# Performance work log

Measured on AMD Instinct MI355X. Metric: run time of the kernel, lower is better.

## Reference

```python
import jax, jax.numpy as jnp
import numpy as np

B, D_MODEL, SEQ = 8, 1024, 1024   # D_MODEL = hidden_dim*2
H, DK, DV = 8, 128, 128
EPS_LN, EPS_NORM, NEG = 1e-6, 1e-12, -1e9


def layer_norm_2d(x, g, b):
    # torch LayerNorm([d_model, seq_len]): normalize over last two dims
    mu = jnp.mean(x, axis=(-2, -1), keepdims=True)
    var = jnp.mean((x - mu) ** 2, axis=(-2, -1), keepdims=True)
    return (x - mu) * jax.lax.rsqrt(var + EPS_LN) * g + b


def setup_inputs() -> dict:
    key = jax.random.key(0)
    ks = jax.random.split(key, 14)
    s = lambda *sh: 1.0 / np.sqrt(sh[-1])
    return {
        "enc_input": jax.random.normal(ks[0], (B, D_MODEL, SEQ), jnp.float32),
        "slf_attn_mask": jax.random.randint(ks[1], (B, D_MODEL, D_MODEL), 0, 2, jnp.int32),
        "ln1_g": jnp.ones((D_MODEL, SEQ), jnp.float32),
        "ln1_b": jnp.zeros((D_MODEL, SEQ), jnp.float32),
        "wq": jax.random.normal(ks[2], (H * DK, SEQ), jnp.float32) * s(SEQ),
        "wk": jax.random.normal(ks[3], (H * DK, SEQ), jnp.float32) * s(SEQ),
        "wv": jax.random.normal(ks[4], (H * DV, SEQ), jnp.float32) * s(SEQ),
        "wo": jax.random.normal(ks[5], (SEQ, H * DV), jnp.float32) * s(H * DV),
        "ln2_g": jnp.ones((D_MODEL, SEQ), jnp.float32),
        "ln2_b": jnp.zeros((D_MODEL, SEQ), jnp.float32),
        "w1": jax.random.normal(ks[6], (SEQ, SEQ), jnp.float32) * s(SEQ),
        "b1": jnp.zeros((SEQ,), jnp.float32),
        "w2": jax.random.normal(ks[7], (SEQ, SEQ), jnp.float32) * s(SEQ),
        "b2": jnp.zeros((SEQ,), jnp.float32),
    }


def reference(enc_input, slf_attn_mask, ln1_g, ln1_b, wq, wk, wv, wo,
              ln2_g, ln2_b, w1, b1, w2, b2):
    x = enc_input                                # [B, M, S], M = d_model
    residual = x
    h = layer_norm_2d(x, ln1_g, ln1_b)
    # linear projections on last (seq) dim, split heads -> [B, H, M, dk]
    q = jnp.einsum('bms,os->bmo', h, wq).reshape(B, D_MODEL, H, DK).transpose(0, 2, 1, 3)
    k = jnp.einsum('bms,os->bmo', h, wk).reshape(B, D_MODEL, H, DK).transpose(0, 2, 1, 3)
    v = jnp.einsum('bms,os->bmo', h, wv).reshape(B, D_MODEL, H, DV).transpose(0, 2, 1, 3)
    # F.normalize over dim=1 (the HEAD axis) -- faithful to source
    k_norm = k / jnp.maximum(jnp.sqrt(jnp.sum(k * k, axis=1, keepdims=True)), EPS_NORM)
    # no temperature scaling (stored but unused in source)
    attn = jnp.einsum('bhmd,bhnd->bhmn', q, k_norm)          # [B, H, M, M]
    attn = jnp.where(slf_attn_mask[:, None] == 0, NEG, attn)
    attn = jax.nn.softmax(attn, axis=-1)
    out = jnp.einsum('bhmn,bhnd->bhmd', attn, v)             # [B, H, M, dv]
    out = out.transpose(0, 2, 1, 3).reshape(B, D_MODEL, H * DV)
    x = jnp.einsum('bmo,so->bms', out, wo) + residual        # fc + residual
    # positionwise FFN on the seq axis, pre-LN residual
    h2 = layer_norm_2d(x, ln2_g, ln2_b)
    h2 = jax.nn.relu(jnp.einsum('bms,os->bmo', h2, w1) + b1)
    h2 = jnp.einsum('bmo,so->bms', h2, w2) + b2
    enc_output = h2 + x
    return enc_output, attn
```

## Files before the change

### kernel.cpp

```cpp
#include <hip/hip_runtime.h>

#define DEVINL __device__ __forceinline__

typedef __bf16 bf16x8 __attribute__((ext_vector_type(8)));
typedef float  f32x4  __attribute__((ext_vector_type(4)));

DEVINL unsigned short f2bf(float f) {
  union { float f; unsigned int u; } v; v.f = f;
  unsigned int u = v.u;
  return (unsigned short)((u + 0x7fffu + ((u >> 16) & 1u)) >> 16);
}
DEVINL float bf2f(unsigned short b) {
  union { unsigned int u; float f; } v; v.u = ((unsigned int)b) << 16;
  return v.f;
}
DEVINL __bf16 fbf(float f) {
  unsigned short u = f2bf(f);
  return __builtin_bit_cast(__bf16, u);
}

#define GLD_LDS16(SRC, DST) \
  __builtin_amdgcn_global_load_lds((const __attribute__((address_space(1))) void*)(SRC), \
                                   (__attribute__((address_space(3))) void*)(DST), 16, 0, 0)

template<int EPI, bool AF32>
__global__ __launch_bounds__(256) void gemm_bt(
    const void* __restrict__ Ap, const unsigned short* __restrict__ Bp, void* __restrict__ Cp,
    const float* __restrict__ bias, const float* __restrict__ res,
    int M, int N, int K, int lda, int ldb, int ldc, int H,
    long sAb, long sAh, long sBb, long sBh, long sCb, long sCh)
{
  constexpr int ABYTES = AF32 ? 16384 : 8192;
  constexpr int SMEMSZ = (EPI == 2) ? 34816 : (ABYTES + 8192);
  __shared__ __align__(16) char smem[SMEMSZ];
  unsigned short* sB = (unsigned short*)(smem + ABYTES);

  const int tid = threadIdx.x;
  const int w = tid >> 6, l = tid & 63;
  const int wr = w >> 1, wc = w & 1;
  const int ntn = N >> 7;
  const int tm = (int)blockIdx.x / ntn;
  const int tn = (int)blockIdx.x - tm * ntn;
  const int z = blockIdx.z;
  const int bb = z / H, hh = z - bb * H;
  const long offA = (long)bb * sAb + (long)hh * sAh;
  const long offB = (long)bb * sBb + (long)hh * sBh;
  const long offC = (long)bb * sCb + (long)hh * sCh;

  f32x4 zero = {0.f, 0.f, 0.f, 0.f};
  f32x4 acc[4][4];
  #pragma unroll
  for (int m = 0; m < 4; ++m)
    #pragma unroll
    for (int n = 0; n < 4; ++n) acc[m][n] = zero;

  for (int k0 = 0; k0 < K; k0 += 32) {
    __syncthreads();
    if constexpr (!AF32) {
      const unsigned short* A = (const unsigned short*)Ap;
      const int rl = l >> 2, cl = (l & 3) << 3;
      #pragma unroll
      for (int i = 0; i < 2; ++i) {
        const unsigned short* src = A + offA + (long)(tm*128 + w*32 + i*16 + rl) * lda + (k0 + cl);
        unsigned short* dst = (unsigned short*)smem + (w*32 + i*16) * 32;
        GLD_LDS16(src, dst);
      }
    } else {
      const float* A = (const float*)Ap;
      const int rl = l >> 3, cl = (l & 7) << 2;
      #pragma unroll
      for (int i = 0; i < 4; ++i) {
        const float* src = A + offA + (long)(tm*128 + w*32 + i*8 + rl) * lda + (k0 + cl);
        float* dst = (float*)smem + (w*32 + i*8) * 32;
        GLD_LDS16(src, dst);
      }
    }
    {
      const int rl = l >> 2, cl = (l & 3) << 3;
      #pragma unroll
      for (int i = 0; i < 2; ++i) {
        const unsigned short* src = Bp + offB + (long)(tn*128 + w*32 + i*16 + rl) * ldb + (k0 + cl);
        unsigned short* dst = sB + (w*32 + i*16) * 32;
        GLD_LDS16(src, dst);
      }
    }
    __syncthreads();

    bf16x8 af[4], bfr[4];
    if constexpr (!AF32) {
      const unsigned short* sA = (const unsigned short*)smem;
      #pragma unroll
      for (int m = 0; m < 4; ++m) {
        int row = wr*64 + m*16 + (l & 15);
        af[m] = *(const bf16x8*)(sA + row*32 + ((l >> 4) << 3));
      }
    } else {
      const float* sA = (const float*)smem;
      #pragma unroll
      for (int m = 0; m < 4; ++m) {
        int row = wr*64 + m*16 + (l & 15);
        const float* p = sA + row*32 + ((l >> 4) << 3);
        f32x4 v0 = *(const f32x4*)p;
        f32x4 v1 = *(const f32x4*)(p + 4);
        bf16x8 t;
        t[0]=fbf(v0[0]); t[1]=fbf(v0[1]); t[2]=fbf(v0[2]); t[3]=fbf(v0[3]);
        t[4]=fbf(v1[0]); t[5]=fbf(v1[1]); t[6]=fbf(v1[2]); t[7]=fbf(v1[3]);
        af[m] = t;
      }
    }
    #pragma unroll
    for (int n = 0; n < 4; ++n) {
      int row = wc*64 + n*16 + (l & 15);
      bfr[n] = *(const bf16x8*)(sB + row*32 + ((l >> 4) << 3));
    }
    #pragma unroll
    for (int m = 0; m < 4; ++m)
      #pragma unroll
      for (int n = 0; n < 4; ++n)
        acc[m][n] = __builtin_amdgcn_mfma_f32_16x16x32_bf16(af[m], bfr[n], acc[m][n], 0, 0, 0);
  }

  if constexpr (EPI == 2) {
    __syncthreads();
    unsigned short* sT = (unsigned short*)smem;
    #pragma unroll
    for (int m = 0; m < 4; ++m)
      #pragma unroll
      for (int n = 0; n < 4; ++n)
        #pragma unroll
        for (int r = 0; r < 4; ++r) {
          int rowl = wr*64 + m*16 + ((l >> 4) << 2) + r;
          int coll = wc*64 + n*16 + (l & 15);
          sT[coll*136 + rowl] = f2bf(acc[m][n][r]);
        }
    __syncthreads();
    #pragma unroll
    for (int i = 0; i < 8; ++i) {
      int idx = tid + i*256;
      int c = idx >> 4, ch = idx & 15;
      bf16x8 vv = *(const bf16x8*)(sT + c*136 + ch*8);
      *(bf16x8*)((unsigned short*)Cp + offC + (long)(tn*128 + c)*ldc + (tm*128 + ch*8)) = vv;
    }
  } else {
    #pragma unroll
    for (int m = 0; m < 4; ++m) {
      #pragma unroll
      for (int n = 0; n < 4; ++n) {
        #pragma unroll
        for (int r = 0; r < 4; ++r) {
          int row = tm*128 + wr*64 + m*16 + ((l >> 4) << 2) + r;
          int col = tn*128 + wc*64 + n*16 + (l & 15);
          float v = acc[m][n][r];
          long ci = offC + (long)row * ldc + col;
          if constexpr (EPI == 1) {
            ((unsigned short*)Cp)[ci] = f2bf(v);
          } else if constexpr (EPI == 3) {
            ((float*)Cp)[ci] = v + res[ci];
          } else if constexpr (EPI == 4) {
            ((unsigned short*)Cp)[ci] = f2bf(fmaxf(v + bias[col], 0.f));
          } else if constexpr (EPI == 5) {
            ((float*)Cp)[ci] = v + bias[col] + res[ci];
          }
        }
      }
    }
  }
}

template<int EPI>
__global__ __launch_bounds__(256) void gemm_split(
    const unsigned short* __restrict__ A1, const unsigned short* __restrict__ A2,
    const unsigned short* __restrict__ B1, const unsigned short* __restrict__ B2,
    void* __restrict__ Cp, unsigned short* __restrict__ Cp2,
    int M, int N, int K, int lda, int ldb, int ldc, int H,
    long sAb, long sAh, long sBb, long sBh, long sCb, long sCh)
{
  __shared__ __align__(16) unsigned short sAll[4 * 4096];
  unsigned short* sA1 = sAll;
  unsigned short* sA2 = sAll + 4096;
  unsigned short* sB1 = sAll + 8192;
  unsigned short* sB2 = sAll + 12288;

  const int tid = threadIdx.x;
  const int w = tid >> 6, l = tid & 63;
  const int wr = w >> 1, wc = w & 1;
  const int ntn = N >> 7;
  const int tm = (int)blockIdx.x / ntn;
  const int tn = (int)blockIdx.x - tm * ntn;
  const int z = blockIdx.z;
  const int bb = z / H, hh = z - bb * H;
  const long offA = (long)bb * sAb + (long)hh * sAh;
  const long offB = (long)bb * sBb + (long)hh * sBh;
  const long offC = (long)bb * sCb + (long)hh * sCh;

  f32x4 zero = {0.f, 0.f, 0.f, 0.f};
  f32x4 acc[4][4];
  #pragma unroll
  for (int m = 0; m < 4; ++m)
    #pragma unroll
    for (int n = 0; n < 4; ++n) acc[m][n] = zero;

  const int rl = l >> 2, cl = (l & 3) << 3;

  for (int k0 = 0; k0 < K; k0 += 32) {
    __syncthreads();
    #pragma unroll
    for (int i = 0; i < 2; ++i) {
      const int row = w*32 + i*16;
      const long asrc = offA + (long)(tm*128 + row + rl) * lda + (k0 + cl);
      const long bsrc = offB + (long)(tn*128 + row + rl) * ldb + (k0 + cl);
      GLD_LDS16(A1 + asrc, sA1 + row*32);
      GLD_LDS16(A2 + asrc, sA2 + row*32);
      GLD_LDS16(B1 + bsrc, sB1 + row*32);
      GLD_LDS16(B2 + bsrc, sB2 + row*32);
    }
    __syncthreads();

    bf16x8 a1[4], a2[4], bb4[4];
    int aoff[4], boff[4];
    #pragma unroll
    for (int m = 0; m < 4; ++m) {
      int row = wr*64 + m*16 + (l & 15);
      aoff[m] = row*32 + ((l >> 4) << 3);
      a1[m] = *(const bf16x8*)(sA1 + aoff[m]);
      a2[m] = *(const bf16x8*)(sA2 + aoff[m]);
    }
    #pragma unroll
    for (int n = 0; n < 4; ++n) {
      int row = wc*64 + n*16 + (l & 15);
      boff[n] = row*32 + ((l >> 4) << 3);
      bb4[n] = *(const bf16x8*)(sB1 + boff[n]);
    }
    #pragma unroll
    for (int m = 0; m < 4; ++m)
      #pragma unroll
      for (int n = 0; n < 4; ++n) {
        acc[m][n] = __builtin_amdgcn_mfma_f32_16x16x32_bf16(a1[m], bb4[n], acc[m][n], 0, 0, 0);
        acc[m][n] = __builtin_amdgcn_mfma_f32_16x16x32_bf16(a2[m], bb4[n], acc[m][n], 0, 0, 0);
      }
    #pragma unroll
    for (int n = 0; n < 4; ++n)
      bb4[n] = *(const bf16x8*)(sB2 + boff[n]);
    #pragma unroll
    for (int m = 0; m < 4; ++m)
      #pragma unroll
      for (int n = 0; n < 4; ++n)
        acc[m][n] = __builtin_amdgcn_mfma_f32_16x16x32_bf16(a1[m], bb4[n], acc[m][n], 0, 0, 0);
  }

  #pragma unroll
  for (int m = 0; m < 4; ++m) {
    #pragma unroll
    for (int n = 0; n < 4; ++n) {
      #pragma unroll
      for (int r = 0; r < 4; ++r) {
        int row = tm*128 + wr*64 + m*16 + ((l >> 4) << 2) + r;
        int col = tn*128 + wc*64 + n*16 + (l & 15);
        float v = acc[m][n][r];
        long ci = offC + (long)row * ldc + col;
        if constexpr (EPI == 0) {
          ((float*)Cp)[ci] = v;
        } else {
          unsigned short hv = f2bf(v);
          ((unsigned short*)Cp)[ci] = hv;
          Cp2[ci] = f2bf(v - bf2f(hv));
        }
      }
    }
  }
}

__global__ __launch_bounds__(256) void ln_stats1(const float* __restrict__ x, float2* __restrict__ part) {
  __shared__ float2 sred[4];
  int b = blockIdx.y, blk = blockIdx.x;
  const float4* xp = (const float4*)(x + (long)b * 1048576 + (long)blk * 8192);
  float s = 0.f, ss = 0.f;
  for (int i = threadIdx.x; i < 2048; i += 256) {
    float4 v = xp[i];
    s  += v.x + v.y + v.z + v.w;
    ss += v.x*v.x + v.y*v.y + v.z*v.z + v.w*v.w;
  }
  #pragma unroll
  for (int o = 32; o; o >>= 1) { s += __shfl_down(s, o, 64); ss += __shfl_down(ss, o, 64); }
  if ((threadIdx.x & 63) == 0) sred[threadIdx.x >> 6] = make_float2(s, ss);
  __syncthreads();
  if (threadIdx.x == 0) {
    float S = 0.f, SS = 0.f;
    #pragma unroll
    for (int j = 0; j < 4; ++j) { S += sred[j].x; SS += sred[j].y; }
    part[b * 128 + blk] = make_float2(S, SS);
  }
}

__global__ __launch_bounds__(128) void ln_stats2(const float2* __restrict__ part, float2* __restrict__ stats,
                                                 float invN, float eps) {
  __shared__ float2 tmp[2];
  int b = blockIdx.x;
  float2 p = part[b * 128 + threadIdx.x];
  float s = p.x, ss = p.y;
  #pragma unroll
  for (int o = 32; o; o >>= 1) { s += __shfl_down(s, o, 64); ss += __shfl_down(ss, o, 64); }
  if ((threadIdx.x & 63) == 0) tmp[threadIdx.x >> 6] = make_float2(s, ss);
  __syncthreads();
  if (threadIdx.x == 0) {
    float S = tmp[0].x + tmp[1].x, SS = tmp[0].y + tmp[1].y;
    float mu = S * invN;
    float var = SS * invN - mu * mu;
    stats[b] = make_float2(mu, rsqrtf(var + eps));
  }
}

template<bool LO>
__global__ __launch_bounds__(256) void ln_apply(const float* __restrict__ x, const float* __restrict__ g,
                                                const float* __restrict__ be, const float2* __restrict__ stats,
                                                unsigned short* __restrict__ hi, unsigned short* __restrict__ lo) {
  long i = (long)blockIdx.x * 256 + threadIdx.x;
  long e = i << 2;
  int b   = (int)(e >> 20);
  int rem = (int)(e & 1048575);
  float2 st = stats[b];
  float4 xv = ((const float4*)x)[i];
  float4 gv = *(const float4*)(g + rem);
  float4 bv = *(const float4*)(be + rem);
  float h0 = (xv.x - st.x) * st.y * gv.x + bv.x;
  float h1 = (xv.y - st.x) * st.y * gv.y + bv.y;
  float h2 = (xv.z - st.x) * st.y * gv.z + bv.z;
  float h3 = (xv.w - st.x) * st.y * gv.w + bv.w;
  ushort4 h;
  h.x = f2bf(h0); h.y = f2bf(h1); h.z = f2bf(h2); h.w = f2bf(h3);
  ((ushort4*)hi)[i] = h;
  if (LO) {
    ushort4 l4;
    l4.x = f2bf(h0 - bf2f(h.x)); l4.y = f2bf(h1 - bf2f(h.y));
    l4.z = f2bf(h2 - bf2f(h.z)); l4.w = f2bf(h3 - bf2f(h.w));
    ((ushort4*)lo)[i] = l4;
  }
}

__global__ __launch_bounds__(256) void split_bf16(const float* __restrict__ src,
                                                  unsigned short* __restrict__ hi,
                                                  unsigned short* __restrict__ lo) {
  long i = (long)blockIdx.x * 256 + threadIdx.x;
  float4 v = ((const float4*)src)[i];
  ushort4 h, l4;
  h.x = f2bf(v.x); l4.x = f2bf(v.x - bf2f(h.x));
  h.y = f2bf(v.y); l4.y = f2bf(v.y - bf2f(h.y));
  h.z = f2bf(v.z); l4.z = f2bf(v.z - bf2f(h.z));
  h.w = f2bf(v.w); l4.w = f2bf(v.w - bf2f(h.w));
  ((ushort4*)hi)[i] = h;
  ((ushort4*)lo)[i] = l4;
}

__global__ __launch_bounds__(256) void cast_bf16(const float* __restrict__ src,
                                                 unsigned short* __restrict__ dst) {
  long i = (long)blockIdx.x * 256 + threadIdx.x;
  float4 v = ((const float4*)src)[i];
  ushort4 h;
  h.x = f2bf(v.x); h.y = f2bf(v.y); h.z = f2bf(v.z); h.w = f2bf(v.w);
  ((ushort4*)dst)[i] = h;
}

__global__ __launch_bounds__(256) void knorm_split2(const unsigned short* __restrict__ k1,
                                                    const unsigned short* __restrict__ k2,
                                                    unsigned short* __restrict__ kn1,
                                                    unsigned short* __restrict__ kn2) {
  int t = blockIdx.x * 256 + threadIdx.x;
  int b = t >> 17;
  int rem = t & 131071;
  int m = rem >> 7;
  int d = rem & 127;
  long base = (long)b * 1048576 + (long)m * 1024 + d;
  float v[8]; float s = 0.f;
  #pragma unroll
  for (int h = 0; h < 8; ++h) {
    v[h] = bf2f(k1[base + h * 128]) + bf2f(k2[base + h * 128]);
    s += v[h] * v[h];
  }
  float rn = 1.f / fmaxf(sqrtf(s), 1e-12f);
  #pragma unroll
  for (int h = 0; h < 8; ++h) {
    float f = v[h] * rn;
    unsigned short hv = f2bf(f);
    kn1[base + h * 128] = hv;
    kn2[base + h * 128] = f2bf(f - bf2f(hv));
  }
}

__global__ __launch_bounds__(256) void softmax_mask(float* __restrict__ attn, const int* __restrict__ mask) {
  __shared__ float sred[8];
  int r = blockIdx.x;
  int b = r >> 13;
  int m = r & 1023;
  float* row = attn + (long)r * 1024;
  const int* mrow = mask + (long)b * 1048576 + (long)m * 1024;
  int i = threadIdx.x;
  float4 v = ((const float4*)row)[i];
  int4 mk = ((const int4*)mrow)[i];
  float x0 = mk.x ? v.x : -1e9f;
  float x1 = mk.y ? v.y : -1e9f;
  float x2 = mk.z ? v.z : -1e9f;
  float x3 = mk.w ? v.w : -1e9f;
  float mx = fmaxf(fmaxf(x0, x1), fmaxf(x2, x3));
  #pragma unroll
  for (int o = 32; o; o >>= 1) mx = fmaxf(mx, __shfl_down(mx, o, 64));
  if ((i & 63) == 0) sred[i >> 6] = mx;
  __syncthreads();
  mx = fmaxf(fmaxf(sred[0], sred[1]), fmaxf(sred[2], sred[3]));
  float e0 = __expf(x0 - mx), e1 = __expf(x1 - mx), e2 = __expf(x2 - mx), e3 = __expf(x3 - mx);
  float s = e0 + e1 + e2 + e3;
  #pragma unroll
  for (int o = 32; o; o >>= 1) s += __shfl_down(s, o, 64);
  if ((i & 63) == 0) sred[4 + (i >> 6)] = s;
  __syncthreads();
  s = sred[4] + sred[5] + sred[6] + sred[7];
  float inv = 1.f / s;
  ((float4*)row)[i] = make_float4(e0 * inv, e1 * inv, e2 * inv, e3 * inv);
}

extern "C" void kernel_launch(void* const* d_in, const int* in_sizes, int n_in,
                              void* d_out, int out_size, void* d_ws, size_t ws_size,
                              hipStream_t stream) {
  const float* enc  = (const float*)d_in[0];
  const int*   mask = (const int*)d_in[1];
  const float* ln1g = (const float*)d_in[2];
  const float* ln1b = (const float*)d_in[3];
  const float* wq   = (const float*)d_in[4];
  const float* wk   = (const float*)d_in[5];
  const float* wv   = (const float*)d_in[6];
  const float* wo   = (const float*)d_in[7];
  const float* ln2g = (const float*)d_in[8];
  const float* ln2b = (const float*)d_in[9];
  const float* w1   = (const float*)d_in[10];
  const float* b1   = (const float*)d_in[11];
  const float* w2   = (const float*)d_in[12];
  const float* b2   = (const float*)d_in[13];

  float* out_enc  = (float*)d_out;
  float* out_attn = out_enc + 8388608;

  const size_t MB = 1ull << 20;
  char* ws = (char*)d_ws;
  unsigned short* h1   = (unsigned short*)(ws + 0 * MB);
  unsigned short* h2   = (unsigned short*)(ws + 16 * MB);
  unsigned short* q1   = (unsigned short*)(ws + 32 * MB);
  unsigned short* q2   = (unsigned short*)(ws + 48 * MB);
  unsigned short* k1r  = (unsigned short*)(ws + 64 * MB);
  unsigned short* k2r  = (unsigned short*)(ws + 80 * MB);
  unsigned short* kn1  = (unsigned short*)(ws + 96 * MB);
  unsigned short* kn2  = (unsigned short*)(ws + 112 * MB);
  unsigned short* vt   = (unsigned short*)(ws + 128 * MB);
  unsigned short* outm = (unsigned short*)(ws + 144 * MB);
  float*          x2f  = (float*)(ws + 160 * MB);
  unsigned short* h2b  = (unsigned short*)(ws + 32 * MB);
  unsigned short* tb   = (unsigned short*)(ws + 48 * MB);
  unsigned short* wq1  = (unsigned short*)(ws + 192 * MB);
  unsigned short* wq2  = (unsigned short*)(ws + 194 * MB);
  unsigned short* wk1  = (unsigned short*)(ws + 196 * MB);
  unsigned short* wk2  = (unsigned short*)(ws + 198 * MB);
  unsigned short* wv1  = (unsigned short*)(ws + 200 * MB);
  unsigned short* wob  = (unsigned short*)(ws + 202 * MB);
  unsigned short* w1b  = (unsigned short*)(ws + 204 * MB);
  unsigned short* w2b  = (unsigned short*)(ws + 206 * MB);
  float2* part  = (float2*)(ws + 208 * MB);
  float2* stats = part + 1024;

  const float invN = 1.f / 1048576.f;

  ln_stats1<<<dim3(128, 8), 256, 0, stream>>>(enc, part);
  ln_stats2<<<dim3(8), 128, 0, stream>>>(part, stats, invN, 1e-6f);
  ln_apply<true><<<dim3(8192), 256, 0, stream>>>(enc, ln1g, ln1b, stats, h1, h2);

  split_bf16<<<dim3(1024), 256, 0, stream>>>(wq, wq1, wq2);
  split_bf16<<<dim3(1024), 256, 0, stream>>>(wk, wk1, wk2);
  cast_bf16 <<<dim3(1024), 256, 0, stream>>>(wv, wv1);
  cast_bf16 <<<dim3(1024), 256, 0, stream>>>(wo, wob);
  cast_bf16 <<<dim3(1024), 256, 0, stream>>>(w1, w1b);
  cast_bf16 <<<dim3(1024), 256, 0, stream>>>(w2, w2b);

  gemm_split<6><<<dim3(512, 1, 1), 256, 0, stream>>>(h1, h2, wq1, wq2, q1, q2,
      8192, 1024, 1024, 1024, 1024, 1024, 1, 0, 0, 0, 0, 0, 0);
  gemm_split<6><<<dim3(512, 1, 1), 256, 0, stream>>>(h1, h2, wk1, wk2, k1r, k2r,
      8192, 1024, 1024, 1024, 1024, 1024, 1, 0, 0, 0, 0, 0, 0);

  gemm_bt<2, false><<<dim3(64, 1, 8), 256, 0, stream>>>(h1, wv1, vt, nullptr, nullptr,
      1024, 1024, 1024, 1024, 1024, 1024, 1, 1048576, 0, 0, 0, 1048576, 0);

  knorm_split2<<<dim3(4096), 256, 0, stream>>>(k1r, k2r, kn1, kn2);

  gemm_split<0><<<dim3(64, 1, 64), 256, 0, stream>>>(q1, q2, kn1, kn2, out_attn, nullptr,
      1024, 1024, 128, 1024, 1024, 1024, 8, 1048576, 128, 1048576, 128, 8388608, 1048576);

  softmax_mask<<<dim3(65536), 256, 0, stream>>>(out_attn, mask);

  gemm_bt<1, true><<<dim3(8, 1, 64), 256, 0, stream>>>(out_attn, vt, outm, nullptr, nullptr,
      1024, 128, 1024, 1024, 1024, 1024, 8, 8388608, 1048576, 1048576, 131072, 1048576, 128);

  gemm_bt<3, false><<<dim3(512, 1, 1), 256, 0, stream>>>(outm, wob, x2f, nullptr, enc,
      8192, 1024, 1024, 1024, 1024, 1024, 1, 0, 0, 0, 0, 0, 0);

  ln_stats1<<<dim3(128, 8), 256, 0, stream>>>(x2f, part);
  ln_stats2<<<dim3(8), 128, 0, stream>>>(part, stats, invN, 1e-6f);
  ln_apply<false><<<dim3(8192), 256, 0, stream>>>(x2f, ln2g, ln2b, stats, h2b, nullptr);

  gemm_bt<4, false><<<dim3(512, 1, 1), 256, 0, stream>>>(h2b, w1b, tb, b1, nullptr,
      8192, 1024, 1024, 1024, 1024, 1024, 1, 0, 0, 0, 0, 0, 0);
  gemm_bt<5, false><<<dim3(512, 1, 1), 256, 0, stream>>>(tb, w2b, out_enc, b2, x2f,
      8192, 1024, 1024, 1024, 1024, 1024, 1, 0, 0, 0, 0, 0, 0);
}
```

Measured before the change: 619.6 us.

## Fuse QK^T, mask-softmax and PV into one attention kernel with bit-packed mask

Replaces the separate score GEMM, softmax_mask pass and fp32-input PV GEMM with one attn_fused kernel. Each block computes a 32-row by 1024-column score strip in registers, applies a mask that is first packed to bits, and does the softmax in registers with cross-wave LDS reductions. It writes the attention probabilities once, then reuses a bf16 copy held in LDS for the PV product with a cross-wave reduction. This removes the fp32 attention re-read and rewrite traffic and the int32 mask reads, but uses heavy register pressure, 64KB of LDS per block, and loads K and V straight from global memory without tiling through LDS.

```diff
diff --git a/kernel.cpp b/kernel.cpp
--- a/kernel.cpp
+++ b/kernel.cpp
@@ -14,26 +14,21 @@
   union { unsigned int u; float f; } v; v.u = ((unsigned int)b) << 16;
   return v.f;
 }
-DEVINL __bf16 fbf(float f) {
-  unsigned short u = f2bf(f);
-  return __builtin_bit_cast(__bf16, u);
-}
 
 #define GLD_LDS16(SRC, DST) \
   __builtin_amdgcn_global_load_lds((const __attribute__((address_space(1))) void*)(SRC), \
                                    (__attribute__((address_space(3))) void*)(DST), 16, 0, 0)
 
-template<int EPI, bool AF32>
+template<int EPI>
 __global__ __launch_bounds__(256) void gemm_bt(
-    const void* __restrict__ Ap, const unsigned short* __restrict__ Bp, void* __restrict__ Cp,
+    const unsigned short* __restrict__ Ap, const unsigned short* __restrict__ Bp, void* __restrict__ Cp,
     const float* __restrict__ bias, const float* __restrict__ res,
     int M, int N, int K, int lda, int ldb, int ldc, int H,
     long sAb, long sAh, long sBb, long sBh, long sCb, long sCh)
 {
-  constexpr int ABYTES = AF32 ? 16384 : 8192;
-  constexpr int SMEMSZ = (EPI == 2) ? 34816 : (ABYTES + 8192);
+  constexpr int SMEMSZ = (EPI == 2) ? 34816 : 16384;
   __shared__ __align__(16) char smem[SMEMSZ];
-  unsigned short* sB = (unsigned short*)(smem + ABYTES);
+  unsigned short* sB = (unsigned short*)(smem + 8192);
 
   const int tid = threadIdx.x;
   const int w = tid >> 6, l = tid & 63;
@@ -56,57 +51,22 @@
 
   for (int k0 = 0; k0 < K; k0 += 32) {
     __syncthreads();
-    if constexpr (!AF32) {
-      const unsigned short* A = (const unsigned short*)Ap;
-      const int rl = l >> 2, cl = (l & 3) << 3;
-      #pragma unroll
-      for (int i = 0; i < 2; ++i) {
-        const unsigned short* src = A + offA + (long)(tm*128 + w*32 + i*16 + rl) * lda + (k0 + cl);
-        unsigned short* dst = (unsigned short*)smem + (w*32 + i*16) * 32;
-        GLD_LDS16(src, dst);
-      }
-    } else {
-      const float* A = (const float*)Ap;
-      const int rl = l >> 3, cl = (l & 7) << 2;
-      #pragma unroll
-      for (int i = 0; i < 4; ++i) {
-        const float* src = A + offA + (long)(tm*128 + w*32 + i*8 + rl) * lda + (k0 + cl);
-        float* dst = (float*)smem + (w*32 + i*8) * 32;
-        GLD_LDS16(src, dst);
-      }
-    }
-    {
-      const int rl = l >> 2, cl = (l & 3) << 3;
-      #pragma unroll
-      for (int i = 0; i < 2; ++i) {
-        const unsigned short* src = Bp + offB + (long)(tn*128 + w*32 + i*16 + rl) * ldb + (k0 + cl);
-        unsigned short* dst = sB + (w*32 + i*16) * 32;
-        GLD_LDS16(src, dst);
-      }
+    const int rl = l >> 2, cl = (l & 3) << 3;
+    #pragma unroll
+    for (int i = 0; i < 2; ++i) {
+      const unsigned short* srcA = Ap + offA + (long)(tm*128 + w*32 + i*16 + rl) * lda + (k0 + cl);
+      GLD_LDS16(srcA, (unsigned short*)smem + (w*32 + i*16) * 32);
+      const unsigned short* srcB = Bp + offB + (long)(tn*128 + w*32 + i*16 + rl) * ldb + (k0 + cl);
+      GLD_LDS16(srcB, sB + (w*32 + i*16) * 32);
     }
     __syncthreads();
 
     bf16x8 af[4], bfr[4];
-    if constexpr (!AF32) {
-      const unsigned short* sA = (const unsigned short*)smem;
-      #pragma unroll
-      for (int m = 0; m < 4; ++m) {
-        int row = wr*64 + m*16 + (l & 15);
-        af[m] = *(const bf16x8*)(sA + row*32 + ((l >> 4) << 3));
-      }
-    } else {
-      const float* sA = (const float*)smem;
-      #pragma unroll
-      for (int m = 0; m < 4; ++m) {
-        int row = wr*64 + m*16 + (l & 15);
-        const float* p = sA + row*32 + ((l >> 4) << 3);
-        f32x4 v0 = *(const f32x4*)p;
-        f32x4 v1 = *(const f32x4*)(p + 4);
-        bf16x8 t;
-        t[0]=fbf(v0[0]); t[1]=fbf(v0[1]); t[2]=fbf(v0[2]); t[3]=fbf(v0[3]);
-        t[4]=fbf(v1[0]); t[5]=fbf(v1[1]); t[6]=fbf(v1[2]); t[7]=fbf(v1[3]);
-        af[m] = t;
-      }
+    const unsigned short* sA = (const unsigned short*)smem;
+    #pragma unroll
+    for (int m = 0; m < 4; ++m) {
+      int row = wr*64 + m*16 + (l & 15);
+      af[m] = *(const bf16x8*)(sA + row*32 + ((l >> 4) << 3));
     }
     #pragma unroll
     for (int n = 0; n < 4; ++n) {
@@ -152,9 +112,7 @@
           int col = tn*128 + wc*64 + n*16 + (l & 15);
           float v = acc[m][n][r];
           long ci = offC + (long)row * ldc + col;
-          if constexpr (EPI == 1) {
-            ((unsigned short*)Cp)[ci] = f2bf(v);
-          } else if constexpr (EPI == 3) {
+          if constexpr (EPI == 3) {
             ((float*)Cp)[ci] = v + res[ci];
           } else if constexpr (EPI == 4) {
             ((unsigned short*)Cp)[ci] = f2bf(fmaxf(v + bias[col], 0.f));
@@ -167,13 +125,11 @@
   }
 }
 
-template<int EPI>
 __global__ __launch_bounds__(256) void gemm_split(
     const unsigned short* __restrict__ A1, const unsigned short* __restrict__ A2,
     const unsigned short* __restrict__ B1, const unsigned short* __restrict__ B2,
-    void* __restrict__ Cp, unsigned short* __restrict__ Cp2,
-    int M, int N, int K, int lda, int ldb, int ldc, int H,
-    long sAb, long sAh, long sBb, long sBh, long sCb, long sCh)
+    unsigned short* __restrict__ Cp, unsigned short* __restrict__ Cp2,
+    int M, int N, int K, int lda, int ldb, int ldc)
 {
   __shared__ __align__(16) unsigned short sAll[4 * 4096];
   unsigned short* sA1 = sAll;
@@ -187,11 +143,6 @@
   const int ntn = N >> 7;
   const int tm = (int)blockIdx.x / ntn;
   const int tn = (int)blockIdx.x - tm * ntn;
-  const int z = blockIdx.z;
-  const int bb = z / H, hh = z - bb * H;
-  const long offA = (long)bb * sAb + (long)hh * sAh;
-  const long offB = (long)bb * sBb + (long)hh * sBh;
-  const long offC = (long)bb * sCb + (long)hh * sCh;
 
   f32x4 zero = {0.f, 0.f, 0.f, 0.f};
   f32x4 acc[4][4];
@@ -207,8 +158,8 @@
     #pragma unroll
     for (int i = 0; i < 2; ++i) {
       const int row = w*32 + i*16;
-      const long asrc = offA + (long)(tm*128 + row + rl) * lda + (k0 + cl);
-      const long bsrc = offB + (long)(tn*128 + row + rl) * ldb + (k0 + cl);
+      const long asrc = (long)(tm*128 + row + rl) * lda + (k0 + cl);
+      const long bsrc = (long)(tn*128 + row + rl) * ldb + (k0 + cl);
       GLD_LDS16(A1 + asrc, sA1 + row*32);
       GLD_LDS16(A2 + asrc, sA2 + row*32);
       GLD_LDS16(B1 + bsrc, sB1 + row*32);
@@ -257,16 +208,213 @@
         int row = tm*128 + wr*64 + m*16 + ((l >> 4) << 2) + r;
         int col = tn*128 + wc*64 + n*16 + (l & 15);
         float v = acc[m][n][r];
-        long ci = offC + (long)row * ldc + col;
-        if constexpr (EPI == 0) {
-          ((float*)Cp)[ci] = v;
-        } else {
-          unsigned short hv = f2bf(v);
-          ((unsigned short*)Cp)[ci] = hv;
-          Cp2[ci] = f2bf(v - bf2f(hv));
-        }
+        long ci = (long)row * ldc + col;
+        unsigned short hv = f2bf(v);
+        Cp[ci] = hv;
+        Cp2[ci] = f2bf(v - bf2f(hv));
       }
     }
+  }
+}
+
+__global__ __launch_bounds__(256, 2) void attn_fused(
+    const unsigned short* __restrict__ q1, const unsigned short* __restrict__ q2,
+    const unsigned short* __restrict__ kn1, const unsigned short* __restrict__ kn2,
+    const unsigned short* __restrict__ vt, const unsigned int* __restrict__ mbits,
+    float* __restrict__ attn, unsigned short* __restrict__ outm)
+{
+  __shared__ __align__(16) char smem[65536];
+  const int tid = threadIdx.x;
+  const int w = tid >> 6, l = tid & 63;
+  const int l15 = l & 15, l4 = l >> 4;
+  const int row0 = (int)blockIdx.x * 32;
+  const int z = (int)blockIdx.z;
+  const int bb = z >> 3, hh = z & 7;
+  const long base = (long)bb * 1048576;
+  const int ocol = hh * 128;
+
+  f32x4 s[2][16];
+  #pragma unroll
+  for (int mf = 0; mf < 2; ++mf)
+    #pragma unroll
+    for (int nf = 0; nf < 16; ++nf) s[mf][nf] = (f32x4){0.f, 0.f, 0.f, 0.f};
+
+  #pragma unroll
+  for (int ks = 0; ks < 4; ++ks) {
+    const int kk = ocol + ks*32 + l4*8;
+    bf16x8 a1[2], a2[2];
+    #pragma unroll
+    for (int mf = 0; mf < 2; ++mf) {
+      long ai = base + (long)(row0 + mf*16 + l15) * 1024 + kk;
+      a1[mf] = *(const bf16x8*)(q1 + ai);
+      a2[mf] = *(const bf16x8*)(q2 + ai);
+    }
+    #pragma unroll
+    for (int nf = 0; nf < 16; ++nf) {
+      long bi = base + (long)(w*256 + nf*16 + l15) * 1024 + kk;
+      bf16x8 b1 = *(const bf16x8*)(kn1 + bi);
+      bf16x8 b2 = *(const bf16x8*)(kn2 + bi);
+      #pragma unroll
+      for (int mf = 0; mf < 2; ++mf) {
+        s[mf][nf] = __builtin_amdgcn_mfma_f32_16x16x32_bf16(a1[mf], b1, s[mf][nf], 0, 0, 0);
+        s[mf][nf] = __builtin_amdgcn_mfma_f32_16x16x32_bf16(a2[mf], b1, s[mf][nf], 0, 0, 0);
+        s[mf][nf] = __builtin_amdgcn_mfma_f32_16x16x32_bf16(a1[mf], b2, s[mf][nf], 0, 0, 0);
+      }
+    }
+  }
+
+  #pragma unroll
+  for (int mf = 0; mf < 2; ++mf) {
+    #pragma unroll
+    for (int r = 0; r < 4; ++r) {
+      int mg = row0 + mf*16 + l4*4 + r;
+      const unsigned int* wrow = mbits + (long)bb*32768 + (long)mg*32 + w*8;
+      unsigned int wd[8];
+      #pragma unroll
+      for (int j = 0; j < 8; ++j) wd[j] = wrow[j];
+      #pragma unroll
+      for (int nf = 0; nf < 16; ++nf) {
+        unsigned int bit = (wd[nf >> 1] >> (((nf & 1) << 4) + l15)) & 1u;
+        if (!bit) s[mf][nf][r] = -1e9f;
+      }
+    }
+  }
+
+  float* red = (float*)smem;
+
+  float mx[2][4];
+  #pragma unroll
+  for (int mf = 0; mf < 2; ++mf)
+    #pragma unroll
+    for (int r = 0; r < 4; ++r) {
+      float m = s[mf][0][r];
+      #pragma unroll
+      for (int nf = 1; nf < 16; ++nf) m = fmaxf(m, s[mf][nf][r]);
+      #pragma unroll
+      for (int o = 1; o < 16; o <<= 1) m = fmaxf(m, __shfl_xor(m, o, 64));
+      mx[mf][r] = m;
+      if (l15 == 0) red[w*32 + mf*16 + l4*4 + r] = m;
+    }
+  __syncthreads();
+  #pragma unroll
+  for (int mf = 0; mf < 2; ++mf)
+    #pragma unroll
+    for (int r = 0; r < 4; ++r) {
+      int ml = mf*16 + l4*4 + r;
+      mx[mf][r] = fmaxf(fmaxf(red[ml], red[32 + ml]), fmaxf(red[64 + ml], red[96 + ml]));
+    }
+  __syncthreads();
+
+  float sm[2][4];
+  #pragma unroll
+  for (int mf = 0; mf < 2; ++mf)
+    #pragma unroll
+    for (int r = 0; r < 4; ++r) sm[mf][r] = 0.f;
+  #pragma unroll
+  for (int mf = 0; mf < 2; ++mf)
+    #pragma unroll
+    for (int nf = 0; nf < 16; ++nf)
+      #pragma unroll
+      for (int r = 0; r < 4; ++r) {
+        float e = __expf(s[mf][nf][r] - mx[mf][r]);
+        s[mf][nf][r] = e;
+        sm[mf][r] += e;
+      }
+  #pragma unroll
+  for (int mf = 0; mf < 2; ++mf)
+    #pragma unroll
+    for (int r = 0; r < 4; ++r) {
+      float t = sm[mf][r];
+      #pragma unroll
+      for (int o = 1; o < 16; o <<= 1) t += __shfl_xor(t, o, 64);
+      if (l15 == 0) red[w*32 + mf*16 + l4*4 + r] = t;
+    }
+  __syncthreads();
+  float inv[2][4];
+  #pragma unroll
+  for (int mf = 0; mf < 2; ++mf)
+    #pragma unroll
+    for (int r = 0; r < 4; ++r) {
+      int ml = mf*16 + l4*4 + r;
+      inv[mf][r] = 1.f / (red[ml] + red[32 + ml] + red[64 + ml] + red[96 + ml]);
+    }
+  __syncthreads();
+
+  char* pbase = smem + w * 16384;
+  float* arow = attn + (long)(bb*8 + hh) * 1048576;
+  #pragma unroll
+  for (int mf = 0; mf < 2; ++mf)
+    #pragma unroll
+    for (int nf = 0; nf < 16; ++nf)
+      #pragma unroll
+      for (int r = 0; r < 4; ++r) {
+        int ml = mf*16 + l4*4 + r;
+        int cl = nf*16 + l15;
+        float a = s[mf][nf][r] * inv[mf][r];
+        arow[(long)(row0 + ml) * 1024 + (w*256 + cl)] = a;
+        int byte = (ml*512 + cl*2) ^ ((ml & 7) << 4);
+        *(unsigned short*)(pbase + byte) = f2bf(a);
+      }
+  __syncthreads();
+
+  f32x4 o[2][8];
+  #pragma unroll
+  for (int mf = 0; mf < 2; ++mf)
+    #pragma unroll
+    for (int df = 0; df < 8; ++df) o[mf][df] = (f32x4){0.f, 0.f, 0.f, 0.f};
+  #pragma unroll
+  for (int ks = 0; ks < 8; ++ks) {
+    bf16x8 pa[2];
+    #pragma unroll
+    for (int mf = 0; mf < 2; ++mf) {
+      int ml = mf*16 + l15;
+      int byte = (ml*512 + (ks*32 + l4*8)*2) ^ ((ml & 7) << 4);
+      pa[mf] = *(const bf16x8*)(pbase + byte);
+    }
+    #pragma unroll
+    for (int df = 0; df < 8; ++df) {
+      long vi = base + (long)(ocol + df*16 + l15) * 1024 + (w*256 + ks*32 + l4*8);
+      bf16x8 vb = *(const bf16x8*)(vt + vi);
+      #pragma unroll
+      for (int mf = 0; mf < 2; ++mf)
+        o[mf][df] = __builtin_amdgcn_mfma_f32_16x16x32_bf16(pa[mf], vb, o[mf][df], 0, 0, 0);
+    }
+  }
+  __syncthreads();
+
+  float* pp = (float*)smem + w * 4096;
+  #pragma unroll
+  for (int mf = 0; mf < 2; ++mf)
+    #pragma unroll
+    for (int df = 0; df < 8; ++df)
+      #pragma unroll
+      for (int r = 0; r < 4; ++r)
+        pp[(mf*16 + l4*4 + r)*128 + df*16 + l15] = o[mf][df][r];
+  __syncthreads();
+  #pragma unroll
+  for (int it = 0; it < 4; ++it) {
+    int i = tid + it*256;
+    f32x4 a4 = ((const f32x4*)smem)[i];
+    a4 += ((const f32x4*)(smem + 16384))[i];
+    a4 += ((const f32x4*)(smem + 32768))[i];
+    a4 += ((const f32x4*)(smem + 49152))[i];
+    int ml = i >> 5, d0 = (i & 31) << 2;
+    ushort4 st;
+    st.x = f2bf(a4[0]); st.y = f2bf(a4[1]); st.z = f2bf(a4[2]); st.w = f2bf(a4[3]);
+    *(ushort4*)(outm + (long)(bb*1024 + row0 + ml) * 1024 + ocol + d0) = st;
+  }
+}
+
+__global__ __launch_bounds__(256) void pack_mask(const int* __restrict__ mask,
+                                                 unsigned int* __restrict__ bits) {
+  int w = threadIdx.x >> 6, l = threadIdx.x & 63;
+  long rowid = (long)blockIdx.x * 4 + w;
+  const int* mrow = mask + rowid * 1024;
+  unsigned int* brow = bits + rowid * 32;
+  #pragma unroll
+  for (int it = 0; it < 16; ++it) {
+    unsigned long long b = __ballot(mrow[it*64 + l] != 0);
+    if (l == 0) { brow[it*2] = (unsigned int)b; brow[it*2 + 1] = (unsigned int)(b >> 32); }
   }
 }
 
@@ -384,37 +532,6 @@
     kn1[base + h * 128] = hv;
     kn2[base + h * 128] = f2bf(f - bf2f(hv));
   }
-}
-
-__global__ __launch_bounds__(256) void softmax_mask(float* __restrict__ attn, const int* __restrict__ mask) {
-  __shared__ float sred[8];
-  int r = blockIdx.x;
-  int b = r >> 13;
-  int m = r & 1023;
-  float* row = attn + (long)r * 1024;
-  const int* mrow = mask + (long)b * 1048576 + (long)m * 1024;
-  int i = threadIdx.x;
-  float4 v = ((const float4*)row)[i];
-  int4 mk = ((const int4*)mrow)[i];
-  float x0 = mk.x ? v.x : -1e9f;
-  float x1 = mk.y ? v.y : -1e9f;
-  float x2 = mk.z ? v.z : -1e9f;
-  float x3 = mk.w ? v.w : -1e9f;
-  float mx = fmaxf(fmaxf(x0, x1), fmaxf(x2, x3));
-  #pragma unroll
-  for (int o = 32; o; o >>= 1) mx = fmaxf(mx, __shfl_down(mx, o, 64));
-  if ((i & 63) == 0) sred[i >> 6] = mx;
-  __syncthreads();
-  mx = fmaxf(fmaxf(sred[0], sred[1]), fmaxf(sred[2], sred[3]));
-  float e0 = __expf(x0 - mx), e1 = __expf(x1 - mx), e2 = __expf(x2 - mx), e3 = __expf(x3 - mx);
-  float s = e0 + e1 + e2 + e3;
-  #pragma unroll
-  for (int o = 32; o; o >>= 1) s += __shfl_down(s, o, 64);
-  if ((i & 63) == 0) sred[4 + (i >> 6)] = s;
-  __syncthreads();
-  s = sred[4] + sred[5] + sred[6] + sred[7];
-  float inv = 1.f / s;
-  ((float4*)row)[i] = make_float4(e0 * inv, e1 * inv, e2 * inv, e3 * inv);
 }
 
 extern "C" void kernel_launch(void* const* d_in, const int* in_sizes, int n_in,
@@ -463,6 +580,7 @@
   unsigned short* w2b  = (unsigned short*)(ws + 206 * MB);
   float2* part  = (float2*)(ws + 208 * MB);
   float2* stats = part + 1024;
+  unsigned int* mbits = (unsigned int*)(ws + 209 * MB);
 
   const float invN = 1.f / 1048576.f;
 
@@ -476,34 +594,27 @@
   cast_bf16 <<<dim3(1024), 256, 0, stream>>>(wo, wob);
   cast_bf16 <<<dim3(1024), 256, 0, stream>>>(w1, w1b);
   cast_bf16 <<<dim3(1024), 256, 0, stream>>>(w2, w2b);
-
-  gemm_split<6><<<dim3(512, 1, 1), 256, 0, stream>>>(h1, h2, wq1, wq2, q1, q2,
-      8192, 1024, 1024, 1024, 1024, 1024, 1, 0, 0, 0, 0, 0, 0);
-  gemm_split<6><<<dim3(512, 1, 1), 256, 0, stream>>>(h1, h2, wk1, wk2, k1r, k2r,
-      8192, 1024, 1024, 1024, 1024, 1024, 1, 0, 0, 0, 0, 0, 0);
-
-  gemm_bt<2, false><<<dim3(64, 1, 8), 256, 0, stream>>>(h1, wv1, vt, nullptr, nullptr,
+  pack_mask <<<dim3(2048), 256, 0, stream>>>(mask, mbits);
+
+  gemm_split<<<dim3(512), 256, 0, stream>>>(h1, h2, wq1, wq2, q1, q2, 8192, 1024, 1024, 1024, 1024, 1024);
+  gemm_split<<<dim3(512), 256, 0, stream>>>(h1, h2, wk1, wk2, k1r, k2r, 8192, 1024, 1024, 1024, 1024, 1024);
+
+  gemm_bt<2><<<dim3(64, 1, 8), 256, 0, stream>>>(h1, wv1, vt, nullptr, nullptr,
       1024, 1024, 1024, 1024, 1024, 1024, 1, 1048576, 0, 0, 0, 1048576, 0);
 
   knorm_split2<<<dim3(4096), 256, 0, stream>>>(k1r, k2r, kn1, kn2);
 
-  gemm_split<0><<<dim3(64, 1, 64), 256, 0, stream>>>(q1, q2, kn1, kn2, out_attn, nullptr,
-      1024, 1024, 128, 1024, 1024, 1024, 8, 1048576, 128, 1048576, 128, 8388608, 1048576);
-
-  softmax_mask<<<dim3(65536), 256, 0, stream>>>(out_attn, mask);
-
-  gemm_bt<1, true><<<dim3(8, 1, 64), 256, 0, stream>>>(out_attn, vt, outm, nullptr, nullptr,
-      1024, 128, 1024, 1024, 1024, 1024, 8, 8388608, 1048576, 1048576, 131072, 1048576, 128);
-
-  gemm_bt<3, false><<<dim3(512, 1, 1), 256, 0, stream>>>(outm, wob, x2f, nullptr, enc,
+  attn_fused<<<dim3(32, 1, 64), 256, 0, stream>>>(q1, q2, kn1, kn2, vt, mbits, out_attn, outm);
+
+  gemm_bt<3><<<dim3(512), 256, 0, stream>>>(outm, wob, x2f, nullptr, enc,
       8192, 1024, 1024, 1024, 1024, 1024, 1, 0, 0, 0, 0, 0, 0);
 
   ln_stats1<<<dim3(128, 8), 256, 0, stream>>>(x2f, part);
   ln_stats2<<<dim3(8), 128, 0, stream>>>(part, stats, invN, 1e-6f);
   ln_apply<false><<<dim3(8192), 256, 0, stream>>>(x2f, ln2g, ln2b, stats, h2b, nullptr);
 
-  gemm_bt<4, false><<<dim3(512, 1, 1), 256, 0, stream>>>(h2b, w1b, tb, b1, nullptr,
+  gemm_bt<4><<<dim3(512), 256, 0, stream>>>(h2b, w1b, tb, b1, nullptr,
       8192, 1024, 1024, 1024, 1024, 1024, 1, 0, 0, 0, 0, 0, 0);
-  gemm_bt<5, false><<<dim3(512, 1, 1), 256, 0, stream>>>(tb, w2b, out_enc, b2, x2f,
+  gemm_bt<5><<<dim3(512), 256, 0, stream>>>(tb, w2b, out_enc, b2, x2f,
       8192, 1024, 1024, 1024, 1024, 1024, 1, 0, 0, 0, 0, 0, 0);
 }
```

Result: no change. 619.9 us (+0.1%).
